# Optimization experiments

Measured on AMD Instinct MI355X. Metric: run time of the kernel, lower is better.

## Reference

```python
import jax, jax.numpy as jnp
import numpy as np

NUM_CLASSES = 1000
FEAT_DIM = 512
K = 2  # centers per class
BATCH = 32768


def setup_inputs() -> dict:
    key = jax.random.key(0)
    k1, k2, k3 = jax.random.split(key, 3)
    x = jax.random.normal(k1, (BATCH, FEAT_DIM), dtype=jnp.float32)
    labels = jax.random.randint(k2, (BATCH,), 0, NUM_CLASSES, dtype=jnp.int64)
    centers = jax.random.normal(k3, (NUM_CLASSES * K, FEAT_DIM), dtype=jnp.float32)
    return {"x": x, "labels": labels, "centers": centers}


def reference(x, labels, centers):
    # centers viewed as [num_classes, K, D]; gather per-sample class centers -> [B, K, D]
    c = centers.reshape(NUM_CLASSES, K, FEAT_DIM)[labels]
    # squared euclidean distance to each of the K centers, then min over K
    d = jnp.sum((x[:, None, :] - c) ** 2, axis=-1)  # [B, K]
    min_d = jnp.min(d, axis=-1)                      # [B]
    return jnp.mean(min_d)
```

## Files before the change

### kernel.cpp

```cpp
#include <hip/hip_runtime.h>

#define BATCH 32768
#define FEAT 512
#define KCENT 2
#define SAMPLES_PER_WAVE 4
#define NBLOCKS (BATCH / (4 * SAMPLES_PER_WAVE))

typedef float vf4 __attribute__((ext_vector_type(4)));

__device__ __forceinline__ vf4 nt_load4(const float* __restrict__ p) {
    return __builtin_nontemporal_load((const vf4*)p);
}

__global__ __launch_bounds__(256) void mcl_partial(
    const float* __restrict__ x,
    const int* __restrict__ labels,
    const float* __restrict__ centers,
    float* __restrict__ partial)
{
    const int wave = threadIdx.x >> 6;
    const int lane = threadIdx.x & 63;
    const int gw   = blockIdx.x * 4 + wave;
    const int base = gw * SAMPLES_PER_WAVE;

    int labv = 0;
    if (lane < SAMPLES_PER_WAVE) labv = labels[base + lane];

    float wsum = 0.f;

#pragma unroll
    for (int s = 0; s < SAMPLES_PER_WAVE; ++s) {
        const int lab = __shfl(labv, s, 64);
        const float* __restrict__ xrow = x + (size_t)(base + s) * FEAT;
        const float* __restrict__ c0   = centers + (size_t)lab * (KCENT * FEAT);

        float d0 = 0.f, d1 = 0.f;
#pragma unroll
        for (int j = 0; j < 2; ++j) {
            const int off = j * 256 + lane * 4;
            const vf4 xv = nt_load4(xrow + off);
            const vf4 a  = *(const vf4*)(c0 + off);
            const vf4 b  = *(const vf4*)(c0 + FEAT + off);
            float e;
            e = xv.x - a.x; d0 += e * e;
            e = xv.y - a.y; d0 += e * e;
            e = xv.z - a.z; d0 += e * e;
            e = xv.w - a.w; d0 += e * e;
            e = xv.x - b.x; d1 += e * e;
            e = xv.y - b.y; d1 += e * e;
            e = xv.z - b.z; d1 += e * e;
            e = xv.w - b.w; d1 += e * e;
        }

#pragma unroll
        for (int sh = 32; sh > 0; sh >>= 1) {
            d0 += __shfl_down(d0, sh, 64);
            d1 += __shfl_down(d1, sh, 64);
        }
        if (lane == 0) wsum += fminf(d0, d1);
    }

    __shared__ float sacc[4];
    if (lane == 0) sacc[wave] = wsum;
    __syncthreads();
    if (threadIdx.x == 0) {
        const float v = (sacc[0] + sacc[1]) + (sacc[2] + sacc[3]);
        __builtin_nontemporal_store(v, &partial[blockIdx.x]);
    }
}

__global__ __launch_bounds__(256) void mcl_final(
    const float* __restrict__ partial, float* __restrict__ out)
{
    float s = 0.f;
#pragma unroll
    for (int j = 0; j < NBLOCKS / 256; ++j)
        s += partial[j * 256 + threadIdx.x];
#pragma unroll
    for (int sh = 32; sh > 0; sh >>= 1) s += __shfl_down(s, sh, 64);
    __shared__ float ws[4];
    const int wave = threadIdx.x >> 6;
    const int lane = threadIdx.x & 63;
    if (lane == 0) ws[wave] = s;
    __syncthreads();
    if (threadIdx.x == 0)
        out[0] = ((ws[0] + ws[1]) + (ws[2] + ws[3])) * (1.0f / (float)BATCH);
}

extern "C" void kernel_launch(void* const* d_in, const int* in_sizes, int n_in,
                              void* d_out, int out_size, void* d_ws, size_t ws_size,
                              hipStream_t stream) {
    const float* x       = (const float*)d_in[0];
    const int*   labels  = (const int*)d_in[1];
    const float* centers = (const float*)d_in[2];
    float* out = (float*)d_out;
    float* partial = (float*)d_ws;

    mcl_partial<<<NBLOCKS, 256, 0, stream>>>(x, labels, centers, partial);
    mcl_final<<<1, 256, 0, stream>>>(partial, out);
}
```

Measured before the change: 112.0 us.

## Split each wave into 16-lane groups processing four samples concurrently

```diff
diff --git a/kernel.cpp b/kernel.cpp
--- a/kernel.cpp
+++ b/kernel.cpp
@@ -3,8 +3,9 @@
 #define BATCH 32768
 #define FEAT 512
 #define KCENT 2
-#define SAMPLES_PER_WAVE 4
-#define NBLOCKS (BATCH / (4 * SAMPLES_PER_WAVE))
+#define SPW 8
+#define WPB 4
+#define NBLOCKS (BATCH / (SPW * WPB))
 
 typedef float vf4 __attribute__((ext_vector_type(4)));
 
@@ -20,24 +21,26 @@
 {
     const int wave = threadIdx.x >> 6;
     const int lane = threadIdx.x & 63;
-    const int gw   = blockIdx.x * 4 + wave;
-    const int base = gw * SAMPLES_PER_WAVE;
+    const int grp  = lane >> 4;
+    const int gl   = lane & 15;
+    const int base = (blockIdx.x * WPB + wave) * SPW;
 
     int labv = 0;
-    if (lane < SAMPLES_PER_WAVE) labv = labels[base + lane];
+    if (lane < SPW) labv = labels[base + lane];
 
-    float wsum = 0.f;
+    float msum = 0.f;
 
 #pragma unroll
-    for (int s = 0; s < SAMPLES_PER_WAVE; ++s) {
-        const int lab = __shfl(labv, s, 64);
-        const float* __restrict__ xrow = x + (size_t)(base + s) * FEAT;
+    for (int r = 0; r < SPW / 4; ++r) {
+        const int smp = r * 4 + grp;
+        const int lab = __shfl(labv, smp, 64);
+        const float* __restrict__ xrow = x + (size_t)(base + smp) * FEAT;
         const float* __restrict__ c0   = centers + (size_t)lab * (KCENT * FEAT);
 
         float d0 = 0.f, d1 = 0.f;
 #pragma unroll
-        for (int j = 0; j < 2; ++j) {
-            const int off = j * 256 + lane * 4;
+        for (int j = 0; j < 8; ++j) {
+            const int off = j * 64 + gl * 4;
             const vf4 xv = nt_load4(xrow + off);
             const vf4 a  = *(const vf4*)(c0 + off);
             const vf4 b  = *(const vf4*)(c0 + FEAT + off);
@@ -53,15 +56,18 @@
         }
 
 #pragma unroll
-        for (int sh = 32; sh > 0; sh >>= 1) {
-            d0 += __shfl_down(d0, sh, 64);
-            d1 += __shfl_down(d1, sh, 64);
+        for (int sh = 1; sh <= 8; sh <<= 1) {
+            d0 += __shfl_xor(d0, sh, 64);
+            d1 += __shfl_xor(d1, sh, 64);
         }
-        if (lane == 0) wsum += fminf(d0, d1);
+        msum += fminf(d0, d1);
     }
 
-    __shared__ float sacc[4];
-    if (lane == 0) sacc[wave] = wsum;
+    msum += __shfl_xor(msum, 16, 64);
+    msum += __shfl_xor(msum, 32, 64);
+
+    __shared__ float sacc[WPB];
+    if (lane == 0) sacc[wave] = msum;
     __syncthreads();
     if (threadIdx.x == 0) {
         const float v = (sacc[0] + sacc[1]) + (sacc[2] + sacc[3]);
```

New measurement: 110.5 us. No clear change (-1.3%).
